# Performance work log

Hardware: AMD Instinct MI355X
Metric: run time of the kernel (lower is better)

## Reference

```python
import jax, jax.numpy as jnp
import numpy as np

N = 262144   # number of samples
C = 16       # GMM components
D = 64       # feature dim


def setup_inputs() -> dict:
    key = jax.random.key(0)
    k1, k2, k3, k4 = jax.random.split(key, 4)
    inputs = jax.random.normal(k1, (N, D), dtype=jnp.float32)
    # SPD inverse covariances, as produced by inverting fitted GMM covariances
    R = jax.random.normal(k2, (C, D, D), dtype=jnp.float32)
    covariances_inv = jnp.einsum('cij,ckj->cik', R, R) / D + 0.1 * jnp.eye(D, dtype=jnp.float32)
    means = jax.random.normal(k3, (C, D), dtype=jnp.float32)
    w = jax.random.uniform(k4, (C,), dtype=jnp.float32, minval=0.1, maxval=1.0)
    weights = w / jnp.sum(w)  # mixture weights sum to 1
    return {"inputs": inputs, "covariances_inv": covariances_inv,
            "means": means, "weights": weights}


def reference(inputs, covariances_inv, means, weights):
    # Mahalanobis quadratic form per component: d[n,c] = (x_n - m_c)^T Sigma_c^{-1} (x_n - m_c)
    centered = inputs[:, None, :] - means[None, :, :]                # [N, C, D]
    distances_sqr = jnp.einsum('ncd,cde,nce->nc', centered, covariances_inv, centered)  # [N, C]
    # score_n = prod_c d[n,c] ** w_c
    score = jnp.prod(distances_sqr ** weights[None, :], axis=1)      # [N]
    return score
```

## Files before the change

### kernel.cpp

```cpp
#include <hip/hip_runtime.h>

typedef __attribute__((ext_vector_type(4))) float f32x4;
typedef __attribute__((ext_vector_type(8))) short bf16x8;

__device__ __forceinline__ short f2bf(float f) {
    union { float f; unsigned u; } v; v.f = f;
    unsigned u = v.u + 0x7FFFu + ((v.u >> 16) & 1u);
    return (short)(u >> 16);
}
__device__ __forceinline__ int pack_bf2(float a, float b) {
    union { float f; unsigned u; } ua, ub; ua.f = a; ub.f = b;
    unsigned x = ua.u + 0x8000u, y = ub.u + 0x8000u;
    return (int)__builtin_amdgcn_perm(y, x, 0x07060302u);
}
__device__ __forceinline__ float bflo(int p) {
    union { int i; float f; } v; v.i = p << 16; return v.f;
}
__device__ __forceinline__ float bfhi(int p) {
    union { int i; float f; } v; v.i = p & 0xffff0000; return v.f;
}

__global__ void gmm_prep(const float* __restrict__ Ainv,
                         const float* __restrict__ means,
                         short* __restrict__ AbP16,
                         float* __restrict__ biasP,
                         float* __restrict__ kscal) {
    __shared__ float sA[64 * 68];
    __shared__ float sm[64];
    __shared__ float sb[64];
    const int c = blockIdx.x, t = threadIdx.x;
    const float* A = Ainv + c * 4096;
    #pragma unroll
    for (int i = 0; i < 4; ++i) {
        int flat = i * 1024 + t * 4;
        int r = flat >> 6, col = flat & 63;
        *(f32x4*)&sA[r * 68 + col] = *(const f32x4*)(A + flat);
    }
    if (t < 64) sm[t] = means[c * 64 + t];
    __syncthreads();
    {
        int j = t >> 2, seg = t & 3;
        float p = 0.f;
        #pragma unroll
        for (int k = 0; k < 16; ++k) p += sA[j * 68 + seg * 16 + k] * sm[seg * 16 + k];
        p += __shfl_xor(p, 1, 64); p += __shfl_xor(p, 2, 64);
        if ((t & 3) == 0) sb[j] = p;
    }
    __syncthreads();
    if (t < 64) {
        float km = sm[t] * sb[t];
        #pragma unroll
        for (int off = 32; off >= 1; off >>= 1) km += __shfl_xor(km, off, 64);
        if (t == 0) kscal[c] = km;
        int rt = t >> 4, qh = (t >> 2) & 3, r = t & 3;
        int pj = (rt >> 1) * 32 + 8 * qh + 4 * (rt & 1) + r;
        biasP[c * 64 + t] = -2.f * sb[pj];
    }
    #pragma unroll
    for (int rep = 0; rep < 2; ++rep) {
        int f = rep * 256 + t;
        int rt = f >> 7, kc = (f >> 6) & 1, L = f & 63;
        int ln = L & 15, q = L >> 4;
        int pj = (rt >> 1) * 32 + 8 * (ln >> 2) + 4 * (rt & 1) + (ln & 3);
        const float* src = &sA[pj * 68 + 32 * kc + 8 * q];
        bf16x8 v;
        #pragma unroll
        for (int j = 0; j < 8; ++j) v[j] = f2bf(src[j]);
        *(bf16x8*)(AbP16 + c * 4096 + f * 8) = v;
    }
}

union BFrag { bf16x8 v; int i[4]; };

__global__ __launch_bounds__(256) void gmm_main(
    const float* __restrict__ X,
    const float* __restrict__ weights,
    const short* __restrict__ AbP16,
    const float* __restrict__ biasP,
    const float* __restrict__ kscal,
    float* __restrict__ out) {

    __shared__ short sAb[16384];
    __shared__ float sBias[16 * 64];
    __shared__ float sKW[32];

    const int tid = threadIdx.x;
    const int lane = tid & 63, w = tid >> 6;
    const int q = lane >> 4, ln = lane & 15;
    const int base = blockIdx.x * 256 + w * 64;

    #pragma unroll
    for (int i = 0; i < 8; ++i)
        ((int4*)sAb)[i * 256 + tid] = ((const int4*)AbP16)[i * 256 + tid];
    ((f32x4*)sBias)[tid] = ((const f32x4*)biasP)[tid];
    if (tid < 16) { sKW[tid] = kscal[tid]; sKW[16 + tid] = weights[tid]; }

    BFrag xb[4][2];
    #pragma unroll
    for (int t = 0; t < 4; ++t) {
        const float* xr = X + (size_t)(base + t * 16 + ln) * 64 + 8 * q;
        #pragma unroll
        for (int kc = 0; kc < 2; ++kc) {
            f32x4 a = *(const f32x4*)(xr + 32 * kc);
            f32x4 b = *(const f32x4*)(xr + 32 * kc + 4);
            xb[t][kc].i[0] = pack_bf2(a[0], a[1]);
            xb[t][kc].i[1] = pack_bf2(a[2], a[3]);
            xb[t][kc].i[2] = pack_bf2(b[0], b[1]);
            xb[t][kc].i[3] = pack_bf2(b[2], b[3]);
        }
    }
    __syncthreads();

    float slog[4] = {0.f, 0.f, 0.f, 0.f};

    #pragma unroll 1
    for (int g = 0; g < 4; ++g) {
        #pragma unroll 1
        for (int cl = 0; cl < 4; ++cl) {
            const int c = g * 4 + cl;
            bf16x8 af[8];
            #pragma unroll
            for (int f = 0; f < 8; ++f)
                af[f] = *(const bf16x8*)&sAb[cl * 4096 + f * 512 + lane * 8];
            f32x4 bias[4];
            #pragma unroll
            for (int rt = 0; rt < 4; ++rt)
                bias[rt] = *(const f32x4*)&sBias[c * 64 + rt * 16 + q * 4];
            const float kc_ = sKW[c], wcc = sKW[16 + c];

            #pragma unroll
            for (int t = 0; t < 4; ++t) {
                float dp = 0.f;
                #pragma unroll
                for (int rt = 0; rt < 4; ++rt) {
                    f32x4 acc = __builtin_amdgcn_mfma_f32_16x16x32_bf16(
                        af[rt * 2 + 0], xb[t][0].v, bias[rt], 0, 0, 0);
                    acc = __builtin_amdgcn_mfma_f32_16x16x32_bf16(
                        af[rt * 2 + 1], xb[t][1].v, acc, 0, 0, 0);
                    int pa = xb[t][rt >> 1].i[(rt & 1) * 2];
                    int pb = xb[t][rt >> 1].i[(rt & 1) * 2 + 1];
                    dp += acc[0] * bflo(pa) + acc[1] * bfhi(pa)
                        + acc[2] * bflo(pb) + acc[3] * bfhi(pb);
                }
                dp += __shfl_xor(dp, 16, 64);
                dp += __shfl_xor(dp, 32, 64);
                float d = fmaxf(dp + kc_, 1e-30f);
                slog[t] = fmaf(wcc, __builtin_amdgcn_logf(d), slog[t]);
            }
        }
        if (g < 3) {
            __syncthreads();
            const int4* src = (const int4*)(AbP16 + (g + 1) * 16384);
            #pragma unroll
            for (int i = 0; i < 8; ++i)
                ((int4*)sAb)[i * 256 + tid] = src[i * 256 + tid];
            __syncthreads();
        }
    }

    if (q == 0) {
        #pragma unroll
        for (int t = 0; t < 4; ++t)
            out[base + t * 16 + ln] = __builtin_amdgcn_exp2f(slog[t]);
    }
}

extern "C" void kernel_launch(void* const* d_in, const int* in_sizes, int n_in,
                              void* d_out, int out_size, void* d_ws, size_t ws_size,
                              hipStream_t stream) {
    const float* X       = (const float*)d_in[0];
    const float* Ainv    = (const float*)d_in[1];
    const float* means   = (const float*)d_in[2];
    const float* weights = (const float*)d_in[3];
    float* out = (float*)d_out;
    const int N = in_sizes[0] / 64;

    short* AbP16 = (short*)d_ws;
    float* biasP = (float*)((char*)d_ws + 131072);
    float* kscal = (float*)((char*)d_ws + 135168);

    gmm_prep<<<dim3(16), dim3(256), 0, stream>>>(Ainv, means, AbP16, biasP, kscal);
    gmm_main<<<dim3(N / 256), dim3(256), 0, stream>>>(X, weights, AbP16, biasP, kscal, out);
}
```

Before: 133.3 us.

## Prefetch next component group into registers, use permlane swaps, spread output stores

Loads the next group of four components' bf16 matrices from global memory into registers at the start of each group, so the load latency overlaps the MFMA work and the shared-memory refill between barriers only writes registers. The cross-lane reduction uses permlane16/32 swap builtins when they are available instead of DPP/LDS shuffles. The dot-product accumulation is split into two independent chains. The final output is written by all 64 lanes with a select instead of only the q==0 lanes. The cost is 32 extra VGPRs per thread for the prefetch buffer, which may lower occupancy.

New measurement: 150.2 us. 12.6% more time.

```diff
diff --git a/kernel.cpp b/kernel.cpp
--- a/kernel.cpp
+++ b/kernel.cpp
@@ -19,6 +19,24 @@
 __device__ __forceinline__ float bfhi(int p) {
     union { int i; float f; } v; v.i = p & 0xffff0000; return v.f;
 }
+
+#if __has_builtin(__builtin_amdgcn_permlane16_swap) && \
+    __has_builtin(__builtin_amdgcn_permlane32_swap)
+__device__ __forceinline__ float quad_sum(float dp) {
+    unsigned u = __float_as_uint(dp);
+    auto r1 = __builtin_amdgcn_permlane16_swap(u, u, false, false);
+    float s = __uint_as_float(r1[0]) + __uint_as_float(r1[1]);
+    unsigned v = __float_as_uint(s);
+    auto r2 = __builtin_amdgcn_permlane32_swap(v, v, false, false);
+    return __uint_as_float(r2[0]) + __uint_as_float(r2[1]);
+}
+#else
+__device__ __forceinline__ float quad_sum(float dp) {
+    dp += __shfl_xor(dp, 16, 64);
+    dp += __shfl_xor(dp, 32, 64);
+    return dp;
+}
+#endif
 
 __global__ void gmm_prep(const float* __restrict__ Ainv,
                          const float* __restrict__ means,
@@ -112,9 +130,15 @@
     __syncthreads();
 
     float slog[4] = {0.f, 0.f, 0.f, 0.f};
+    int4 pf[8];
 
     #pragma unroll 1
     for (int g = 0; g < 4; ++g) {
+        if (g < 3) {
+            const int4* src = (const int4*)(AbP16 + (g + 1) * 16384);
+            #pragma unroll
+            for (int i = 0; i < 8; ++i) pf[i] = src[i * 256 + tid];
+        }
         #pragma unroll 1
         for (int cl = 0; cl < 4; ++cl) {
             const int c = g * 4 + cl;
@@ -130,7 +154,7 @@
 
             #pragma unroll
             for (int t = 0; t < 4; ++t) {
-                float dp = 0.f;
+                float dp0 = 0.f, dp1 = 0.f;
                 #pragma unroll
                 for (int rt = 0; rt < 4; ++rt) {
                     f32x4 acc = __builtin_amdgcn_mfma_f32_16x16x32_bf16(
@@ -139,30 +163,28 @@
                         af[rt * 2 + 1], xb[t][1].v, acc, 0, 0, 0);
                     int pa = xb[t][rt >> 1].i[(rt & 1) * 2];
                     int pb = xb[t][rt >> 1].i[(rt & 1) * 2 + 1];
-                    dp += acc[0] * bflo(pa) + acc[1] * bfhi(pa)
-                        + acc[2] * bflo(pb) + acc[3] * bfhi(pb);
+                    float pr = acc[0] * bflo(pa) + acc[1] * bfhi(pa)
+                             + acc[2] * bflo(pb) + acc[3] * bfhi(pb);
+                    if (rt & 1) dp1 += pr; else dp0 += pr;
                 }
-                dp += __shfl_xor(dp, 16, 64);
-                dp += __shfl_xor(dp, 32, 64);
+                float dp = quad_sum(dp0 + dp1);
                 float d = fmaxf(dp + kc_, 1e-30f);
                 slog[t] = fmaf(wcc, __builtin_amdgcn_logf(d), slog[t]);
             }
         }
         if (g < 3) {
             __syncthreads();
-            const int4* src = (const int4*)(AbP16 + (g + 1) * 16384);
             #pragma unroll
             for (int i = 0; i < 8; ++i)
-                ((int4*)sAb)[i * 256 + tid] = src[i * 256 + tid];
+                ((int4*)sAb)[i * 256 + tid] = pf[i];
             __syncthreads();
         }
     }
 
-    if (q == 0) {
-        #pragma unroll
-        for (int t = 0; t < 4; ++t)
-            out[base + t * 16 + ln] = __builtin_amdgcn_exp2f(slog[t]);
-    }
+    float s0 = (q & 1) ? slog[1] : slog[0];
+    float s1 = (q & 1) ? slog[3] : slog[2];
+    float sv = (q & 2) ? s1 : s0;
+    out[base + lane] = __builtin_amdgcn_exp2f(sv);
 }
 
 extern "C" void kernel_launch(void* const* d_in, const int* in_sizes, int n_in,
```
